# Performance work log

Hardware: AMD Instinct MI355X
Metric: run time of the kernel (lower is better)

## Reference

```python
import jax, jax.numpy as jnp
import numpy as np

OUT_SIZE, K0, K_MIN, K_MAX = 7, 4, 2, 5


def setup_inputs() -> dict:
    key = jax.random.key(0)
    ks = jax.random.split(key, 8)
    B, C, H, W, K = 4, 256, 800, 800, 512
    p2 = jax.random.normal(ks[0], (B, C, 200, 200), jnp.float32)
    p3 = jax.random.normal(ks[1], (B, C, 100, 100), jnp.float32)
    p4 = jax.random.normal(ks[2], (B, C, 50, 50), jnp.float32)
    p5 = jax.random.normal(ks[3], (B, C, 25, 25), jnp.float32)
    # boxes: centers uniform in image, sizes log-uniform in [16, 512] px
    cx = jax.random.uniform(ks[4], (B, K)) * W
    cy = jax.random.uniform(ks[5], (B, K)) * H
    logs = jax.random.uniform(ks[6], (B, K, 2), minval=np.log(16.0), maxval=np.log(512.0))
    wh = jnp.exp(logs)
    x1 = jnp.clip(cx - wh[..., 0] * 0.5, 0.0, W - 1.0)
    x2 = jnp.clip(cx + wh[..., 0] * 0.5, 0.0, float(W))
    y1 = jnp.clip(cy - wh[..., 1] * 0.5, 0.0, H - 1.0)
    y2 = jnp.clip(cy + wh[..., 1] * 0.5, 0.0, float(H))
    proposals = jnp.stack([x1, y1, jnp.maximum(x2, x1 + 1.0), jnp.maximum(y2, y1 + 1.0)], axis=-1)
    return {"p2": p2, "p3": p3, "p4": p4, "p5": p5, "proposals": proposals, "H": H, "W": W}


def _bilinear_border(fm_nhwc, b_idx, gx, gy):
    """grid_sample(mode=bilinear, align_corners=True, padding_mode=border).
    fm_nhwc: [B,Hf,Wf,C]; b_idx: [N]; gx,gy: [N,S,S] in [-1,1]. -> [N,S,S,C]"""
    Hf, Wf = fm_nhwc.shape[1], fm_nhwc.shape[2]
    x = jnp.clip((gx + 1.0) * 0.5 * (Wf - 1), 0.0, Wf - 1.0)
    y = jnp.clip((gy + 1.0) * 0.5 * (Hf - 1), 0.0, Hf - 1.0)
    x0 = jnp.floor(x)
    y0 = jnp.floor(y)
    wx = x - x0
    wy = y - y0
    xi0 = x0.astype(jnp.int32)
    yi0 = y0.astype(jnp.int32)
    xi1 = jnp.minimum(xi0 + 1, Wf - 1)
    yi1 = jnp.minimum(yi0 + 1, Hf - 1)
    b = b_idx[:, None, None]
    v00 = fm_nhwc[b, yi0, xi0]  # [N,S,S,C]
    v01 = fm_nhwc[b, yi0, xi1]
    v10 = fm_nhwc[b, yi1, xi0]
    v11 = fm_nhwc[b, yi1, xi1]
    wx = wx[..., None]
    wy = wy[..., None]
    top = v00 * (1.0 - wx) + v01 * wx
    bot = v10 * (1.0 - wx) + v11 * wx
    return top * (1.0 - wy) + bot * wy


def reference(p2, p3, p4, p5, proposals, H, W):
    B, K, _ = proposals.shape
    boxes = proposals.reshape(-1, 4)  # [N,4]
    N = boxes.shape[0]
    b_idx = jnp.repeat(jnp.arange(B, dtype=jnp.int32), K)
    # FPN level assignment: k = floor(k0 + log2(sqrt(area)/224)) clamped
    areas = jnp.sqrt(jnp.clip((boxes[:, 2] - boxes[:, 0]) * (boxes[:, 3] - boxes[:, 1]), 1e-6))
    lev = jnp.clip(jnp.floor(K0 + jnp.log2(areas / 224.0)), K_MIN, K_MAX).astype(jnp.int32) - K_MIN
    # normalized box corners in [-1,1]
    x1n = boxes[:, 0] / W * 2.0 - 1.0
    y1n = boxes[:, 1] / H * 2.0 - 1.0
    x2n = boxes[:, 2] / W * 2.0 - 1.0
    y2n = boxes[:, 3] / H * 2.0 - 1.0
    g = jnp.linspace(0.0, 1.0, OUT_SIZE)
    gy_g, gx_g = jnp.meshgrid(g, g, indexing="ij")  # [S,S]
    gx = x1n[:, None, None] + (x2n - x1n)[:, None, None] * gx_g[None]
    gy = y1n[:, None, None] + (y2n - y1n)[:, None, None] * gy_g[None]
    C = p2.shape[1]
    out = jnp.zeros((N, OUT_SIZE, OUT_SIZE, C), p2.dtype)
    for lvl, fm in enumerate([p2, p3, p4, p5]):
        crop = _bilinear_border(fm.transpose(0, 2, 3, 1), b_idx, gx, gy)
        out = out + jnp.where((lev == lvl)[:, None, None, None], crop, 0.0)
    return out.transpose(0, 3, 1, 2)  # [N,C,S,S]
```

## Files before the change

### kernel.cpp

```cpp
#include <hip/hip_runtime.h>

#define OUT_S 7
#define NPTS  49
#define C_CH  256

__global__ __launch_bounds__(256, 8) void roi_align_fused(
    const float* __restrict__ p2, const float* __restrict__ p3,
    const float* __restrict__ p4, const float* __restrict__ p5,
    const float* __restrict__ prop, const int* __restrict__ Hp,
    const int* __restrict__ Wp, float* __restrict__ out, int K_per_img)
{
    const int n    = blockIdx.x;
    const int lane = threadIdx.x & 63;
    const int wave = threadIdx.x >> 6;
    const int b    = n / K_per_img;

    const float W = (float)Wp[0];
    const float H = (float)Hp[0];

    const float4 box = reinterpret_cast<const float4*>(prop)[n];
    const float x1 = box.x, y1 = box.y, x2 = box.z, y2 = box.w;

    const float area = fmaxf((x2 - x1) * (y2 - y1), 1e-6f);
    const float sqa  = sqrtf(area);
    int lev = (int)floorf(4.0f + log2f(sqa / 224.0f));
    lev = min(max(lev, 2), 5);

    const float* fm; int Hf, Wf;
    if      (lev == 2) { fm = p2; Hf = 200; Wf = 200; }
    else if (lev == 3) { fm = p3; Hf = 100; Wf = 100; }
    else if (lev == 4) { fm = p4; Hf = 50;  Wf = 50;  }
    else               { fm = p5; Hf = 25;  Wf = 25;  }

    if (lane >= NPTS) return;
    const int iy = lane / OUT_S;
    const int ix = lane - iy * OUT_S;

    const float x1n = x1 / W * 2.0f - 1.0f;
    const float x2n = x2 / W * 2.0f - 1.0f;
    const float y1n = y1 / H * 2.0f - 1.0f;
    const float y2n = y2 / H * 2.0f - 1.0f;
    const float tx = (float)ix * (1.0f / 6.0f);
    const float ty = (float)iy * (1.0f / 6.0f);
    const float gx = x1n + (x2n - x1n) * tx;
    const float gy = y1n + (y2n - y1n) * ty;

    float x = (gx + 1.0f) * 0.5f * (float)(Wf - 1);
    float y = (gy + 1.0f) * 0.5f * (float)(Hf - 1);
    x = fminf(fmaxf(x, 0.0f), (float)(Wf - 1));
    y = fminf(fmaxf(y, 0.0f), (float)(Hf - 1));

    const float x0f = floorf(x), y0f = floorf(y);
    const float wx = x - x0f,  wy = y - y0f;
    const int xi0 = (int)x0f,  yi0 = (int)y0f;
    const int xi1 = min(xi0 + 1, Wf - 1);
    const int yi1 = min(yi0 + 1, Hf - 1);

    const float omwx = 1.0f - wx, omwy = 1.0f - wy;

    const int plane = Hf * Wf;
    const float* base = fm + ((size_t)b * C_CH + (size_t)(wave * 64)) * (size_t)plane;
    float*       op   = out + ((size_t)n * C_CH + (size_t)(wave * 64)) * NPTS + lane;

    int o00 = yi0 * Wf + xi0;
    int o01 = yi0 * Wf + xi1;
    int o10 = yi1 * Wf + xi0;
    int o11 = yi1 * Wf + xi1;

    #pragma unroll 4
    for (int k = 0; k < 64; ++k) {
        const float v00 = base[o00];
        const float v01 = base[o01];
        const float v10 = base[o10];
        const float v11 = base[o11];
        o00 += plane; o01 += plane; o10 += plane; o11 += plane;
        const float top = v00 * omwx + v01 * wx;
        const float bot = v10 * omwx + v11 * wx;
        const float r   = top * omwy + bot * wy;
        __builtin_nontemporal_store(r, &op[(size_t)k * NPTS]);
    }
}

extern "C" void kernel_launch(void* const* d_in, const int* in_sizes, int n_in,
                              void* d_out, int out_size, void* d_ws, size_t ws_size,
                              hipStream_t stream) {
    const float* p2   = (const float*)d_in[0];
    const float* p3   = (const float*)d_in[1];
    const float* p4   = (const float*)d_in[2];
    const float* p5   = (const float*)d_in[3];
    const float* prop = (const float*)d_in[4];
    const int*   Hp   = (const int*)d_in[5];
    const int*   Wp   = (const int*)d_in[6];
    float* out = (float*)d_out;

    const int N = in_sizes[4] / 4;
    const int B = in_sizes[0] / (C_CH * 200 * 200);
    const int K = N / (B > 0 ? B : 1);

    roi_align_fused<<<N, 256, 0, stream>>>(p2, p3, p4, p5, prop, Hp, Wp, out, K);
}
```

Baseline: 401.4 us.

## Flatten channel×point work across all threads and swizzle blocks per XCD

Replaces the per-wave layout, where 15 of 64 lanes sat idle, with a flat index over all 256×49 output elements per ROI. Sample offsets and weights are computed once into shared memory and looked up per element. Output stores become fully contiguous. A block-index remap groups consecutive ROIs onto the same XCD for L2 locality, at the cost of a __syncthreads, LDS lookups and an integer divide per element.

```diff
diff --git a/kernel.cpp b/kernel.cpp
--- a/kernel.cpp
+++ b/kernel.cpp
@@ -3,6 +3,9 @@
 #define OUT_S 7
 #define NPTS  49
 #define C_CH  256
+#define ELEMS (C_CH * NPTS)
+#define ITERS (ELEMS / 256)
+#define NXCD  8
 
 __global__ __launch_bounds__(256, 8) void roi_align_fused(
     const float* __restrict__ p2, const float* __restrict__ p3,
@@ -10,10 +13,18 @@
     const float* __restrict__ prop, const int* __restrict__ Hp,
     const int* __restrict__ Wp, float* __restrict__ out, int K_per_img)
 {
-    const int n    = blockIdx.x;
-    const int lane = threadIdx.x & 63;
-    const int wave = threadIdx.x >> 6;
-    const int b    = n / K_per_img;
+    __shared__ int4   s_off[NPTS];
+    __shared__ float2 s_w[NPTS];
+
+    const int nwg = gridDim.x;
+    int n = blockIdx.x;
+    if ((nwg & (NXCD - 1)) == 0) {
+        const int q = nwg >> 3;
+        n = (n & (NXCD - 1)) * q + (n >> 3);
+    }
+
+    const int t = threadIdx.x;
+    const int b = n / K_per_img;
 
     const float W = (float)Wp[0];
     const float H = (float)Hp[0];
@@ -31,53 +42,62 @@
     else if (lev == 3) { fm = p3; Hf = 100; Wf = 100; }
     else if (lev == 4) { fm = p4; Hf = 50;  Wf = 50;  }
     else               { fm = p5; Hf = 25;  Wf = 25;  }
+    const int plane = Hf * Wf;
 
-    if (lane >= NPTS) return;
-    const int iy = lane / OUT_S;
-    const int ix = lane - iy * OUT_S;
+    if (t < NPTS) {
+        const int iy = t / OUT_S;
+        const int ix = t - iy * OUT_S;
 
-    const float x1n = x1 / W * 2.0f - 1.0f;
-    const float x2n = x2 / W * 2.0f - 1.0f;
-    const float y1n = y1 / H * 2.0f - 1.0f;
-    const float y2n = y2 / H * 2.0f - 1.0f;
-    const float tx = (float)ix * (1.0f / 6.0f);
-    const float ty = (float)iy * (1.0f / 6.0f);
-    const float gx = x1n + (x2n - x1n) * tx;
-    const float gy = y1n + (y2n - y1n) * ty;
+        const float x1n = x1 / W * 2.0f - 1.0f;
+        const float x2n = x2 / W * 2.0f - 1.0f;
+        const float y1n = y1 / H * 2.0f - 1.0f;
+        const float y2n = y2 / H * 2.0f - 1.0f;
+        const float tx = (float)ix * (1.0f / 6.0f);
+        const float ty = (float)iy * (1.0f / 6.0f);
+        const float gx = x1n + (x2n - x1n) * tx;
+        const float gy = y1n + (y2n - y1n) * ty;
 
-    float x = (gx + 1.0f) * 0.5f * (float)(Wf - 1);
-    float y = (gy + 1.0f) * 0.5f * (float)(Hf - 1);
-    x = fminf(fmaxf(x, 0.0f), (float)(Wf - 1));
-    y = fminf(fmaxf(y, 0.0f), (float)(Hf - 1));
+        float x = (gx + 1.0f) * 0.5f * (float)(Wf - 1);
+        float y = (gy + 1.0f) * 0.5f * (float)(Hf - 1);
+        x = fminf(fmaxf(x, 0.0f), (float)(Wf - 1));
+        y = fminf(fmaxf(y, 0.0f), (float)(Hf - 1));
 
-    const float x0f = floorf(x), y0f = floorf(y);
-    const float wx = x - x0f,  wy = y - y0f;
-    const int xi0 = (int)x0f,  yi0 = (int)y0f;
-    const int xi1 = min(xi0 + 1, Wf - 1);
-    const int yi1 = min(yi0 + 1, Hf - 1);
+        const float x0f = floorf(x), y0f = floorf(y);
+        const float wx = x - x0f,  wy = y - y0f;
+        const int xi0 = (int)x0f,  yi0 = (int)y0f;
+        const int xi1 = min(xi0 + 1, Wf - 1);
+        const int yi1 = min(yi0 + 1, Hf - 1);
 
-    const float omwx = 1.0f - wx, omwy = 1.0f - wy;
+        s_off[t] = make_int4(yi0 * Wf + xi0, yi0 * Wf + xi1,
+                             yi1 * Wf + xi0, yi1 * Wf + xi1);
+        s_w[t]   = make_float2(wx, wy);
+    }
+    __syncthreads();
 
-    const int plane = Hf * Wf;
-    const float* base = fm + ((size_t)b * C_CH + (size_t)(wave * 64)) * (size_t)plane;
-    float*       op   = out + ((size_t)n * C_CH + (size_t)(wave * 64)) * NPTS + lane;
-
-    int o00 = yi0 * Wf + xi0;
-    int o01 = yi0 * Wf + xi1;
-    int o10 = yi1 * Wf + xi0;
-    int o11 = yi1 * Wf + xi1;
+    const float* basep = fm + (size_t)b * C_CH * (size_t)plane;
+    float*       outp  = out + (size_t)n * ELEMS;
 
     #pragma unroll 4
-    for (int k = 0; k < 64; ++k) {
-        const float v00 = base[o00];
-        const float v01 = base[o01];
-        const float v10 = base[o10];
-        const float v11 = base[o11];
-        o00 += plane; o01 += plane; o10 += plane; o11 += plane;
-        const float top = v00 * omwx + v01 * wx;
-        const float bot = v10 * omwx + v11 * wx;
-        const float r   = top * omwy + bot * wy;
-        __builtin_nontemporal_store(r, &op[(size_t)k * NPTS]);
+    for (int j = 0; j < ITERS; ++j) {
+        const int idx = t + 256 * j;
+        const int c   = (unsigned)idx / NPTS;
+        const int p   = idx - c * NPTS;
+
+        const int4   o = s_off[p];
+        const float2 w = s_w[p];
+
+        const float* pb = basep + (size_t)c * plane;
+        const float v00 = pb[o.x];
+        const float v01 = pb[o.y];
+        const float v10 = pb[o.z];
+        const float v11 = pb[o.w];
+
+        const float omwx = 1.0f - w.x, omwy = 1.0f - w.y;
+        const float top = v00 * omwx + v01 * w.x;
+        const float bot = v10 * omwx + v11 * w.x;
+        const float r   = top * omwy + bot * w.y;
+
+        __builtin_nontemporal_store(r, &outp[idx]);
     }
 }
 
```

New measurement: 404.1 us. About the same (+0.7%).
